# Kernel tuning notes

Measured on AMD Instinct MI355X. Metric: run time of the kernel, lower is better.

Reference implementation:

```python
import jax, jax.numpy as jnp
import numpy as np

DIM = 1536
NH = 12
HD = DIM // NH  # 128
FF, HH, WW = 32, 8, 12
L = FF * HH * WW  # 3072
WIN = (8, 4, 4)  # block of 128 tokens
BLK = WIN[0] * WIN[1] * WIN[2]


def rms_norm(x, g, eps=1e-5):
    # matches RMSNorm: normalize in fp32, scale by weight
    v = jnp.mean(jnp.square(x), axis=-1, keepdims=True)
    return x * jax.lax.rsqrt(v + eps) * g


def rope(x, freqs, n):
    # x: [B,S,D]; freqs: [S,1,HD/2,2] (cos,sin); complex rotation on pairs
    B, S, D = x.shape
    xr = x.reshape(B, S, n, D // n // 2, 2)
    c, s = freqs[..., 0], freqs[..., 1]        # [S,1,HD/2] broadcast over B,n
    a, b = xr[..., 0], xr[..., 1]
    out = jnp.stack([a * c - b * s, a * s + b * c], axis=-1)
    return out.reshape(B, S, D)


def partition3d(x, f, h, w):
    # [B,f,h,w,D] -> [B, nblocks, 128, D], block order (f/8, h/4, w/4)
    B, D = x.shape[0], x.shape[-1]
    wf, wh, ww = WIN
    x = x.reshape(B, f // wf, wf, h // wh, wh, w // ww, ww, D)
    x = x.transpose(0, 1, 3, 5, 2, 4, 6, 7)
    return x.reshape(B, -1, BLK, D)


def reverse3d(xw, f, h, w):
    # [B, nblocks, 128, D] -> [B, f*h*w, D]
    B, D = xw.shape[0], xw.shape[-1]
    wf, wh, ww = WIN
    x = xw.reshape(B, f // wf, h // wh, w // ww, wf, wh, ww, D)
    x = x.transpose(0, 1, 4, 2, 5, 3, 6, 7)
    return x.reshape(B, f * h * w, D)


def block_mask(f, h, w):
    # build_local_block_mask_3d: spatial mask is all-ones; temporal = context|local
    seqlen = f // WIN[0]
    nb_sp = (h // WIN[1]) * (w // WIN[2])
    stride = WIN[0]
    ctx_idx = (6 + stride - 1) // stride - 1          # context_frames=6
    radius = (5 + stride - 1) // stride               # temp_window_frames=5
    t = jnp.arange(seqlen)
    mt = (t[None, :] <= ctx_idx) | (jnp.abs(t[:, None] - t[None, :]) <= radius)
    # expand temporal block mask over spatial blocks -> [nb, nb]
    return jnp.repeat(jnp.repeat(mt, nb_sp, axis=0), nb_sp, axis=1)


def setup_inputs() -> dict:
    key = jax.random.key(0)
    ks = jax.random.split(key, 8)
    x = jax.random.normal(ks[0], (1, L, DIM), jnp.float32)
    ang = jax.random.uniform(ks[1], (L, 1, HD // 2), jnp.float32, 0.0, 2.0 * np.pi)
    freqs = jnp.stack([jnp.cos(ang), jnp.sin(ang)], axis=-1)  # [L,1,64,2]
    sc = 1.0 / np.sqrt(DIM)
    Wq = jax.random.normal(ks[2], (DIM, DIM), jnp.float32) * sc
    Wk = jax.random.normal(ks[3], (DIM, DIM), jnp.float32) * sc
    Wv = jax.random.normal(ks[4], (DIM, DIM), jnp.float32) * sc
    Wo = jax.random.normal(ks[5], (DIM, DIM), jnp.float32) * sc
    zeros = jnp.zeros((DIM,), jnp.float32)
    ones = jnp.ones((DIM,), jnp.float32)
    return {"x": x, "freqs": freqs, "Wq": Wq, "bq": zeros, "Wk": Wk, "bk": zeros,
            "Wv": Wv, "bv": zeros, "Wo": Wo, "bo": zeros, "g_q": ones, "g_k": ones,
            "f": FF, "h": HH, "w": WW, "local_range": 18}


def reference(x, freqs, Wq, bq, Wk, bk, Wv, bv, Wo, bo, g_q, g_k, f, h, w, local_range):
    B, S, D = x.shape
    q = rms_norm(x @ Wq + bq, g_q, eps=1e-5)
    k = rms_norm(x @ Wk + bk, g_k, eps=1e-5)
    v = x @ Wv + bv
    q = rope(q, freqs, NH)
    k = rope(k, freqs, NH)
    # window partition and flatten back to a reordered sequence
    qs = partition3d(q.reshape(B, f, h, w, D), f, h, w).reshape(B, S, D)
    ks_ = partition3d(k.reshape(B, f, h, w, D), f, h, w).reshape(B, S, D)
    vs = partition3d(v.reshape(B, f, h, w, D), f, h, w).reshape(B, S, D)
    bm = block_mask(f, h, w)                       # [nb, nb] bool
    tok_mask = jnp.repeat(jnp.repeat(bm, BLK, 0), BLK, 1)  # [S, S]
    qh = qs.reshape(B, S, NH, HD).transpose(0, 2, 1, 3)
    kh = ks_.reshape(B, S, NH, HD).transpose(0, 2, 1, 3)
    vh = vs.reshape(B, S, NH, HD).transpose(0, 2, 1, 3)
    scores = jnp.einsum('bhqd,bhkd->bhqk', qh, kh) / np.sqrt(HD)
    scores = jnp.where(tok_mask[None, None], scores, -jnp.inf)
    attn = jax.nn.softmax(scores, axis=-1)
    out = jnp.einsum('bhqk,bhkd->bhqd', attn, vh)
    out = out.transpose(0, 2, 1, 3).reshape(B, S, D)
    out = reverse3d(out.reshape(B, -1, BLK, D), f, h, w)  # undo window reorder
    return out @ Wo + bo
```

## Files before the change

kernel.cpp:

```cpp
#include <hip/hip_runtime.h>
#include <hip/hip_bf16.h>
#include <math.h>

#define S_LEN 3072
#define DMODEL 1536
#define NQKV 4608
#define NHEAD 12
#define HDIM 128
#define NSPLIT 4

typedef __attribute__((ext_vector_type(8))) short bf16x8;
typedef __attribute__((ext_vector_type(4))) float f32x4;
typedef __attribute__((ext_vector_type(4))) unsigned int u32x4;

__device__ __forceinline__ void gload_lds16(const void* g, void* lds) {
  __builtin_amdgcn_global_load_lds(
      (const __attribute__((address_space(1))) unsigned int*)g,
      (__attribute__((address_space(3))) unsigned int*)lds, 16, 0, 0);
}

__device__ __forceinline__ int invperm(int p) {
  int blk = p >> 7;
  int w   = p & 127;
  int fb  = blk / 6;
  int rem = blk - fb * 6;
  int hb  = rem / 3;
  int wb  = rem - hb * 3;
  int fi  = fb * 8 + (w >> 4);
  int hi  = hb * 4 + ((w >> 2) & 3);
  int wi  = wb * 4 + (w & 3);
  return (fi * 8 + hi) * 12 + wi;
}

__device__ __forceinline__ int fwdperm(int s) {
  int fi = s / 96;
  int rem = s - fi * 96;
  int hi = rem / 12;
  int wi = rem - hi * 12;
  int fb = fi >> 3, wf = fi & 7;
  int hb = hi >> 2, wh = hi & 3;
  int wb = wi >> 2, ww = wi & 3;
  return ((fb * 2 + hb) * 3 + wb) * 128 + wf * 16 + wh * 4 + ww;
}

__device__ __forceinline__ void store_out(float* p, float v) { *p = v; }
__device__ __forceinline__ void store_out(__hip_bfloat16* p, float v) { *p = __float2bfloat16(v); }

__global__ __launch_bounds__(256) void convert_bias(
    const float* __restrict__ in, __hip_bfloat16* __restrict__ out,
    const float* __restrict__ bq, const float* __restrict__ bk,
    const float* __restrict__ bv, float* __restrict__ bqkv)
{
  if (blockIdx.x < 4608) {
    int i = blockIdx.x * 256 + threadIdx.x;
    float4 v = ((const float4*)in)[i];
    __hip_bfloat16 b[4] = {__float2bfloat16(v.x), __float2bfloat16(v.y),
                           __float2bfloat16(v.z), __float2bfloat16(v.w)};
    ((ushort4*)out)[i] = *(ushort4*)b;
  } else {
    int j = (blockIdx.x - 4608) * 256 + threadIdx.x;
    float v = (j < 1536) ? bq[j] : (j < 3072) ? bk[j - 1536] : bv[j - 3072];
    bqkv[j] = v;
  }
}

__global__ __launch_bounds__(256) void transpose_convert4(
    const float* __restrict__ W0, const float* __restrict__ W1,
    const float* __restrict__ W2, const float* __restrict__ W3,
    __hip_bfloat16* __restrict__ Wtqkv, __hip_bfloat16* __restrict__ Wot)
{
  __shared__ __hip_bfloat16 Ls[64][67];
  const int z = blockIdx.z;
  const float* W = (z == 0) ? W0 : (z == 1) ? W1 : (z == 2) ? W2 : W3;
  __hip_bfloat16* Wt = (z < 3) ? Wtqkv + (size_t)z * DMODEL * DMODEL : Wot;
  const int r0 = blockIdx.y * 64, c0 = blockIdx.x * 64, t = threadIdx.x;
  {
    int rr = t >> 2, cb = (t & 3) * 16;
    const float4* src = (const float4*)(W + (size_t)(r0 + rr) * DMODEL + c0 + cb);
    #pragma unroll
    for (int i = 0; i < 4; ++i) {
      float4 v = src[i];
      Ls[rr][cb + i * 4 + 0] = __float2bfloat16(v.x);
      Ls[rr][cb + i * 4 + 1] = __float2bfloat16(v.y);
      Ls[rr][cb + i * 4 + 2] = __float2bfloat16(v.z);
      Ls[rr][cb + i * 4 + 3] = __float2bfloat16(v.w);
    }
  }
  __syncthreads();
  {
    int cc = t >> 2, rb = (t & 3) * 16;
    unsigned short tmp[16];
    #pragma unroll
    for (int i = 0; i < 16; ++i) tmp[i] = *(unsigned short*)&Ls[rb + i][cc];
    uint4* dst = (uint4*)(Wt + (size_t)(c0 + cc) * DMODEL + r0 + rb);
    dst[0] = ((uint4*)tmp)[0];
    dst[1] = ((uint4*)tmp)[1];
  }
}

template <typename OutT, int BN>
__global__ __launch_bounds__(256) void gemm_bt(
    const __hip_bfloat16* __restrict__ A, const __hip_bfloat16* __restrict__ Bt,
    const float* __restrict__ bias, OutT* __restrict__ C, int M, int N, int K)
{
  constexpr int NB = BN / 32;
  __shared__ __hip_bfloat16 As[2][128 * 32];
  __shared__ __hip_bfloat16 Bs[2][BN * 32];
  const int tid = threadIdx.x, lane = tid & 63, wid = tid >> 6;
  const int l15 = lane & 15, l4 = lane >> 4;
  const int nwg = gridDim.x * gridDim.y;
  const int lin = blockIdx.y * gridDim.x + blockIdx.x;
  const int cpx = nwg >> 3;
  const int swz = (lin & 7) * cpx + (lin >> 3);
  const int row0 = (swz / gridDim.x) * 128, col0 = (swz % gridDim.x) * BN;
  const int wr = (wid >> 1) * 64, wc = (wid & 1) * (BN / 2);

  f32x4 acc[4][NB] = {};
  const char* Ab = (const char*)A;
  const char* Bb = (const char*)Bt;

  auto STAGE = [&](int buf, int k0) {
    #pragma unroll
    for (int i = 0; i < 2; ++i) {
      int slot = i * 256 + tid;
      int r = slot >> 2;
      int b = (slot & 3) * 16;
      gload_lds16(Ab + ((size_t)(row0 + r) * K + k0) * 2 + b,
                  (char*)As[buf] + ((size_t)i * 256 + wid * 64) * 16);
    }
    #pragma unroll
    for (int i = 0; i < BN / 64; ++i) {
      int slot = i * 256 + tid;
      int r = slot >> 2;
      int b = (slot & 3) * 16;
      gload_lds16(Bb + ((size_t)(col0 + r) * K + k0) * 2 + b,
                  (char*)Bs[buf] + ((size_t)i * 256 + wid * 64) * 16);
    }
  };

  STAGE(0, 0);
  __syncthreads();
  int cur = 0;
  for (int k0 = 0; k0 < K; k0 += 32) {
    if (k0 + 32 < K) STAGE(cur ^ 1, k0 + 32);
    bf16x8 a[4], b[NB];
    #pragma unroll
    for (int m = 0; m < 4; ++m)
      a[m] = *(const bf16x8*)&As[cur][(wr + m * 16 + l15) * 32 + l4 * 8];
    #pragma unroll
    for (int n = 0; n < NB; ++n)
      b[n] = *(const bf16x8*)&Bs[cur][(wc + n * 16 + l15) * 32 + l4 * 8];
    #pragma unroll
    for (int m = 0; m < 4; ++m)
      #pragma unroll
      for (int n = 0; n < NB; ++n)
        acc[m][n] = __builtin_amdgcn_mfma_f32_16x16x32_bf16(a[m], b[n], acc[m][n], 0, 0, 0);
    __syncthreads();
    cur ^= 1;
  }

  #pragma unroll
  for (int m = 0; m < 4; ++m) {
    #pragma unroll
    for (int r = 0; r < 4; ++r) {
      size_t row = row0 + wr + m * 16 + l4 * 4 + r;
      #pragma unroll
      for (int n = 0; n < NB; ++n) {
        int col = col0 + wc + n * 16 + l15;
        store_out(&C[row * N + col], acc[m][n][r] + bias[col]);
      }
    }
  }
}

__global__ __launch_bounds__(256) void norm_rope_perm(
    const __hip_bfloat16* __restrict__ X,
    const float* __restrict__ gq, const float* __restrict__ gk,
    const float* __restrict__ freqs,
    __hip_bfloat16* __restrict__ OutQ, __hip_bfloat16* __restrict__ OutK)
{
  const int s = blockIdx.x, tid = threadIdx.x;
  const int sec = blockIdx.y;
  const float* g = sec ? gk : gq;
  __hip_bfloat16* Out = sec ? OutK : OutQ;
  const float qsc = sec ? 1.0f : (0.08838834764831843f * 1.4426950408889634f);
  const unsigned int* row = (const unsigned int*)(X + (size_t)s * NQKV + sec * 1536);
  float e0[3], e1[3];
  float ss = 0.f;
  #pragma unroll
  for (int i = 0; i < 3; ++i) {
    unsigned int u = row[tid + i * 256];
    float a = __uint_as_float(u << 16);
    float b = __uint_as_float(u & 0xffff0000u);
    e0[i] = a; e1[i] = b;
    ss += a * a + b * b;
  }
  #pragma unroll
  for (int off = 32; off > 0; off >>= 1) ss += __shfl_down(ss, off, 64);
  __shared__ float wsum[4];
  if ((tid & 63) == 0) wsum[tid >> 6] = ss;
  __syncthreads();
  float rs = rsqrtf((wsum[0] + wsum[1] + wsum[2] + wsum[3]) * (1.f / DMODEL) + 1e-5f);
  rs *= qsc;
  const int p = fwdperm(s);
  #pragma unroll
  for (int i = 0; i < 3; ++i) {
    int pi = tid + i * 256;
    int n = pi >> 6, d2 = pi & 63;
    float c  = freqs[(size_t)s * 128 + 2 * d2];
    float sn = freqs[(size_t)s * 128 + 2 * d2 + 1];
    float y0 = e0[i] * rs * g[2 * pi];
    float y1 = e1[i] * rs * g[2 * pi + 1];
    float o0 = y0 * c - y1 * sn;
    float o1 = y0 * sn + y1 * c;
    __hip_bfloat16 b0 = __float2bfloat16(o0), b1 = __float2bfloat16(o1);
    unsigned int u = ((unsigned int)(*(unsigned short*)&b1) << 16) | (*(unsigned short*)&b0);
    ((unsigned int*)Out)[(((size_t)n * S_LEN + p) * HDIM + 2 * d2) >> 1] = u;
  }
}

__global__ __launch_bounds__(256) void v_transpose(
    const __hip_bfloat16* __restrict__ Vsec, __hip_bfloat16* __restrict__ Vt)
{
  __shared__ __hip_bfloat16 Ls[64][136];
  const int p0 = blockIdx.x * 64, h = blockIdx.y, t = threadIdx.x;
  {
    int pl = t & 63, dg = t >> 6;
    int sidx = invperm(p0 + pl);
    const uint4* src = (const uint4*)(Vsec + (size_t)sidx * NQKV + h * HDIM + dg * 32);
    #pragma unroll
    for (int i = 0; i < 4; ++i) {
      uint4 v = src[i];
      *(uint4*)&Ls[pl][dg * 32 + i * 8] = v;
    }
  }
  __syncthreads();
  {
    int d = t >> 1, ph = t & 1;
    unsigned short tmp[32];
    #pragma unroll
    for (int i = 0; i < 32; ++i) tmp[i] = *(unsigned short*)&Ls[ph * 32 + i][d];
    uint4* dst = (uint4*)(Vt + ((size_t)h * HDIM + d) * S_LEN + p0 + ph * 32);
    #pragma unroll
    for (int i = 0; i < 4; ++i) dst[i] = ((uint4*)tmp)[i];
  }
}

__global__ __launch_bounds__(512) void attn_mfma(
    const __hip_bfloat16* __restrict__ Qp, const __hip_bfloat16* __restrict__ Kp,
    const __hip_bfloat16* __restrict__ Vt,
    __hip_bfloat16* __restrict__ Opart, float* __restrict__ ml)
{
  __shared__ __hip_bfloat16 Ks[64 * 128];
  __shared__ __hip_bfloat16 Vs[128 * 64];

  const int hw = blockIdx.x + 24 * (blockIdx.y + NSPLIT * blockIdx.z);
  const int L  = (hw & 7) * 144 + (hw >> 3);
  const int j  = L % 6;
  const int t4 = (L / 6) & 3;
  const int sh = L / 24;
  const int h  = sh % 12;
  const int split = sh / 12;
  const int tg = (t4 == 0) ? 2 : (t4 == 1) ? 1 : (t4 == 2) ? 3 : 0;
  const int qb = tg * 6 + j;

  const int tid = threadIdx.x, lane = tid & 63, wid = tid >> 6;
  const int l15 = lane & 15, l4 = lane >> 4;

  const int NCh = (tg == 0) ? 6 : (tg == 2) ? 12 : 9;
  const int cbegin = split * NCh, cend = cbegin + NCh;

  const char* Kh = (const char*)(Kp + (size_t)h * S_LEN * HDIM);
  const char* Vh = (const char*)(Vt + (size_t)h * HDIM * S_LEN);

  const int kbase = 8 * (l15 >> 2) + (l15 & 3);
  const int ksw = (((l15 & 3) | (((l15 >> 2) & 1) << 2))) << 4;

  unsigned int koffA, voffA;
  {
    unsigned int kr = tid >> 4;
    unsigned int sig = (kr & 3) | (((kr >> 3) & 1) << 2);
    koffA = kr * 256 + (((tid & 15) * 16) ^ (sig << 4));
    unsigned int vr = tid >> 3;
    voffA = vr * (S_LEN * 2) + (((tid & 7) * 16) ^ ((vr & 7) << 4));
  }

  auto k0_of = [&](int ci) { return ci * 64 + ((tg == 3 && ci >= 12) ? 768 : 0); };
  auto STAGE = [&](int k0) {
    const char* ks = Kh + (size_t)k0 * 256;
    gload_lds16(ks + koffA,        (char*)Ks + tid * 16);
    gload_lds16(ks + koffA + 8192, (char*)Ks + tid * 16 + 8192);
    const char* vs = Vh + (size_t)k0 * 2 + voffA;
    gload_lds16(vs,                          (char*)Vs + tid * 16);
    gload_lds16(vs + (size_t)64 * S_LEN * 2, (char*)Vs + tid * 16 + 8192);
  };

  bf16x8 aq[4];
  {
    const __hip_bfloat16* qr = Qp + (size_t)h * S_LEN * HDIM
        + (size_t)(qb * 128 + wid * 16 + l15) * HDIM + l4 * 8;
    #pragma unroll
    for (int dc = 0; dc < 4; ++dc) aq[dc] = *(const bf16x8*)(qr + dc * 32);
  }

  f32x4 oacc[8] = {};
  float m2 = -1e30f;
  float lsum = 0.f;

  for (int ci = cbegin; ci < cend; ++ci) {
    const int k0 = k0_of(ci);
    STAGE(k0);
    __syncthreads();

    f32x4 sfr[4] = {};
    #pragma unroll
    for (int ct = 0; ct < 4; ++ct) {
      int key = kbase + (ct >> 1) * 32 + (ct & 1) * 4;
      #pragma unroll
      for (int dc = 0; dc < 4; ++dc) {
        int b = (dc * 64 + l4 * 16) ^ ksw;
        bf16x8 kf = *(const bf16x8*)((const char*)Ks + key * 256 + b);
        sfr[ct] = __builtin_amdgcn_mfma_f32_16x16x32_bf16(kf, aq[dc], sfr[ct], 0, 0, 0);
      }
    }
    float lmax = fmaxf(
        fmaxf(fmaxf(sfr[0][0], sfr[0][1]), fmaxf(sfr[0][2], sfr[0][3])),
        fmaxf(fmaxf(fmaxf(sfr[1][0], sfr[1][1]), fmaxf(sfr[1][2], sfr[1][3])),
              fmaxf(fmaxf(fmaxf(sfr[2][0], sfr[2][1]), fmaxf(sfr[2][2], sfr[2][3])),
                    fmaxf(fmaxf(sfr[3][0], sfr[3][1]), fmaxf(sfr[3][2], sfr[3][3])))));
    bool grow = lmax > m2 + 8.f;
    if (ci == cbegin || __any(grow)) {
      float mf = lmax;
      mf = fmaxf(mf, __shfl_xor(mf, 16, 64));
      mf = fmaxf(mf, __shfl_xor(mf, 32, 64));
      float mn = fmaxf(m2, mf);
      float corr = exp2f(m2 - mn);
      m2 = mn;
      lsum *= corr;
      float cr[4];
      #pragma unroll
      for (int r = 0; r < 4; ++r) cr[r] = __shfl(corr, l4 * 4 + r, 64);
      #pragma unroll
      for (int n = 0; n < 8; ++n)
        #pragma unroll
        for (int r = 0; r < 4; ++r) oacc[n][r] *= cr[r];
    }
    #pragma unroll
    for (int ct = 0; ct < 4; ++ct)
      #pragma unroll
      for (int r = 0; r < 4; ++r) {
        float p = exp2f(sfr[ct][r] - m2);
        sfr[ct][r] = p;
        lsum += p;
      }
    #pragma unroll
    for (int ks = 0; ks < 2; ++ks) {
      u32x4 wv;
      {
        __hip_bfloat16 a0 = __float2bfloat16(sfr[2 * ks][0]);
        __hip_bfloat16 a1 = __float2bfloat16(sfr[2 * ks][1]);
        __hip_bfloat16 a2 = __float2bfloat16(sfr[2 * ks][2]);
        __hip_bfloat16 a3 = __float2bfloat16(sfr[2 * ks][3]);
        __hip_bfloat16 b0 = __float2bfloat16(sfr[2 * ks + 1][0]);
        __hip_bfloat16 b1 = __float2bfloat16(sfr[2 * ks + 1][1]);
        __hip_bfloat16 b2 = __float2bfloat16(sfr[2 * ks + 1][2]);
        __hip_bfloat16 b3 = __float2bfloat16(sfr[2 * ks + 1][3]);
        wv[0] = ((unsigned int)(*(unsigned short*)&a1) << 16) | (*(unsigned short*)&a0);
        wv[1] = ((unsigned int)(*(unsigned short*)&a3) << 16) | (*(unsigned short*)&a2);
        wv[2] = ((unsigned int)(*(unsigned short*)&b1) << 16) | (*(unsigned short*)&b0);
        wv[3] = ((unsigned int)(*(unsigned short*)&b3) << 16) | (*(unsigned short*)&b2);
      }
      bf16x8 pa = __builtin_bit_cast(bf16x8, wv);
      #pragma unroll
      for (int n = 0; n < 8; ++n) {
        int d = n * 16 + l15;
        int b = (ks * 64 + l4 * 16) ^ ((d & 7) << 4);
        bf16x8 bv = *(const bf16x8*)((const char*)Vs + d * 128 + b);
        oacc[n] = __builtin_amdgcn_mfma_f32_16x16x32_bf16(pa, bv, oacc[n], 0, 0, 0);
      }
    }
    __syncthreads();
  }

  float t = lsum;
  t += __shfl_xor(t, 16, 64);
  t += __shfl_xor(t, 32, 64);
  float inv = 1.0f / t;
  #pragma unroll
  for (int r = 0; r < 4; ++r) {
    float invr = __shfl(inv, l4 * 4 + r, 64);
    int qrow = qb * 128 + wid * 16 + l4 * 4 + r;
    size_t rowid = (size_t)(split * NHEAD + h) * S_LEN + qrow;
    __hip_bfloat16* dst = Opart + rowid * HDIM;
    #pragma unroll
    for (int n = 0; n < 8; ++n)
      dst[n * 16 + l15] = __float2bfloat16(oacc[n][r] * invr);
  }
  if (lane < 16) {
    int qrow = qb * 128 + wid * 16 + lane;
    size_t rowid = (size_t)(split * NHEAD + h) * S_LEN + qrow;
    ml[rowid * 2 + 0] = m2;
    ml[rowid * 2 + 1] = t;
  }
}

__global__ __launch_bounds__(256) void attn_merge(
    const __hip_bfloat16* __restrict__ Opart, const float* __restrict__ ml,
    __hip_bfloat16* __restrict__ AO)
{
  const int rid = blockIdx.x * 4 + (threadIdx.x >> 6);
  const int lane = threadIdx.x & 63;
  const int h = rid / S_LEN, q = rid - h * S_LEN;
  size_t rr[NSPLIT];
  float m[NSPLIT], l[NSPLIT];
  float mm = -1e30f;
  #pragma unroll
  for (int s = 0; s < NSPLIT; ++s) {
    rr[s] = (size_t)(s * NHEAD + h) * S_LEN + q;
    m[s] = ml[rr[s] * 2];
    l[s] = ml[rr[s] * 2 + 1];
    mm = fmaxf(mm, m[s]);
  }
  float wsum = 0.f, wgt[NSPLIT];
  #pragma unroll
  for (int s = 0; s < NSPLIT; ++s) { wgt[s] = l[s] * exp2f(m[s] - mm); wsum += wgt[s]; }
  float inv = 1.0f / wsum;
  float o0 = 0.f, o1 = 0.f;
  #pragma unroll
  for (int s = 0; s < NSPLIT; ++s) {
    unsigned int u = ((const unsigned int*)(Opart + rr[s] * HDIM))[lane];
    float a = wgt[s] * inv;
    o0 += a * __uint_as_float(u << 16);
    o1 += a * __uint_as_float(u & 0xffff0000u);
  }
  __hip_bfloat16 b0 = __float2bfloat16(o0), b1 = __float2bfloat16(o1);
  unsigned int u = ((unsigned int)(*(unsigned short*)&b1) << 16) | (*(unsigned short*)&b0);
  int sorig = invperm(q);
  ((unsigned int*)(AO + (size_t)sorig * DMODEL + h * HDIM))[lane] = u;
}

extern "C" void kernel_launch(void* const* d_in, const int* in_sizes, int n_in,
                              void* d_out, int out_size, void* d_ws, size_t ws_size,
                              hipStream_t stream)
{
  (void)in_sizes; (void)n_in; (void)out_size; (void)ws_size;
  const float* x     = (const float*)d_in[0];
  const float* freqs = (const float*)d_in[1];
  const float* Wq    = (const float*)d_in[2];
  const float* bq    = (const float*)d_in[3];
  const float* Wk    = (const float*)d_in[4];
  const float* bk    = (const float*)d_in[5];
  const float* Wv    = (const float*)d_in[6];
  const float* bv    = (const float*)d_in[7];
  const float* Wo    = (const float*)d_in[8];
  const float* bo    = (const float*)d_in[9];
  const float* gq    = (const float*)d_in[10];
  const float* gk    = (const float*)d_in[11];
  float* out = (float*)d_out;

  char* w = (char*)d_ws;
  __hip_bfloat16* xbf    = (__hip_bfloat16*)(w);
  __hip_bfloat16* Wtqkv  = (__hip_bfloat16*)(w + 9437184);
  __hip_bfloat16* QKVbf  = (__hip_bfloat16*)(w + 23592960);
  __hip_bfloat16* Qp     = (__hip_bfloat16*)(w + 51904512);
  __hip_bfloat16* Kp     = (__hip_bfloat16*)(w + 61341696);
  __hip_bfloat16* Vtb    = (__hip_bfloat16*)(w + 70778880);
  __hip_bfloat16* AO     = (__hip_bfloat16*)(w + 80216064);
  __hip_bfloat16* Wot    = (__hip_bfloat16*)(w + 89653248);
  float*          bqkv   = (float*)(w + 94371840);
  __hip_bfloat16* Opart  = (__hip_bfloat16*)(w + 9437184);
  float*          mlbuf  = (float*)(w);

  hipLaunchKernelGGL(convert_bias, dim3(4626), dim3(256), 0, stream,
                     x, xbf, bq, bk, bv, bqkv);
  hipLaunchKernelGGL(transpose_convert4, dim3(24, 24, 4), dim3(256), 0, stream,
                     Wq, Wk, Wv, Wo, Wtqkv, Wot);

  hipLaunchKernelGGL((gemm_bt<__hip_bfloat16, 128>), dim3(NQKV / 128, S_LEN / 128),
                     dim3(256), 0, stream, xbf, Wtqkv, bqkv, QKVbf, S_LEN, NQKV, DMODEL);

  hipLaunchKernelGGL(norm_rope_perm, dim3(S_LEN, 2), dim3(256), 0, stream,
                     QKVbf, gq, gk, freqs, Qp, Kp);
  hipLaunchKernelGGL(v_transpose, dim3(48, 12), dim3(256), 0, stream, QKVbf + 3072, Vtb);

  hipLaunchKernelGGL(attn_mfma, dim3(24, NSPLIT, NHEAD), dim3(512), 0, stream,
                     Qp, Kp, Vtb, Opart, mlbuf);
  hipLaunchKernelGGL(attn_merge, dim3(S_LEN * NHEAD / 4), dim3(256), 0, stream,
                     Opart, mlbuf, AO);

  hipLaunchKernelGGL((gemm_bt<float, 64>), dim3(DMODEL / 64, S_LEN / 128),
                     dim3(256), 0, stream, AO, Wot, bo, out, S_LEN, DMODEL, DMODEL);
}
```

Measured before the change: 227.9 us.

## Retile QKV GEMM, remap XCD swizzle, relax GEMM barriers, prioritize attention MFMA

The GEMM workgroup mapping now gives each XCD a contiguous 2D sub-tile of the output grid, which should improve L2 reuse. The per-iteration __syncthreads is replaced with partial s_waitcnt vmcnt plus raw barriers, so the next stage's loads can stay in flight while the current tile is consumed. The QKV GEMM switches from 128-wide to 64-wide N tiles to launch more workgroups. The attention kernel raises wave priority around its MFMA blocks with s_setprio. The vmcnt counts are hand-tuned to the number of loads per stage, so they are fragile, and the mapping assumes grid dimensions divisible by 4 and 2.

```diff
diff --git a/kernel.cpp b/kernel.cpp
--- a/kernel.cpp
+++ b/kernel.cpp
@@ -108,11 +108,12 @@
   __shared__ __hip_bfloat16 Bs[2][BN * 32];
   const int tid = threadIdx.x, lane = tid & 63, wid = tid >> 6;
   const int l15 = lane & 15, l4 = lane >> 4;
-  const int nwg = gridDim.x * gridDim.y;
   const int lin = blockIdx.y * gridDim.x + blockIdx.x;
-  const int cpx = nwg >> 3;
-  const int swz = (lin & 7) * cpx + (lin >> 3);
-  const int row0 = (swz / gridDim.x) * 128, col0 = (swz % gridDim.x) * BN;
+  const int xcd = lin & 7, idx = lin >> 3;
+  const int CX = gridDim.x >> 2, CY = gridDim.y >> 1;
+  const int cx = xcd & 3, cy = xcd >> 2;
+  const int lc = idx % CX, lr = idx / CX;
+  const int row0 = (cy * CY + lr) * 128, col0 = (cx * CX + lc) * BN;
   const int wr = (wid >> 1) * 64, wc = (wid & 1) * (BN / 2);
 
   f32x4 acc[4][NB] = {};
@@ -139,10 +140,21 @@
   };
 
   STAGE(0, 0);
-  __syncthreads();
+  asm volatile("s_waitcnt vmcnt(0)" ::: "memory");
+  __builtin_amdgcn_s_barrier();
+  __builtin_amdgcn_sched_barrier(0);
+
   int cur = 0;
   for (int k0 = 0; k0 < K; k0 += 32) {
-    if (k0 + 32 < K) STAGE(cur ^ 1, k0 + 32);
+    if (k0 + 32 < K) {
+      STAGE(cur ^ 1, k0 + 32);
+      if constexpr (BN == 64)
+        asm volatile("s_waitcnt vmcnt(3)" ::: "memory");
+      else
+        asm volatile("s_waitcnt vmcnt(4)" ::: "memory");
+      __builtin_amdgcn_s_barrier();
+    }
+    __builtin_amdgcn_sched_barrier(0);
     bf16x8 a[4], b[NB];
     #pragma unroll
     for (int m = 0; m < 4; ++m)
@@ -155,7 +167,8 @@
       #pragma unroll
       for (int n = 0; n < NB; ++n)
         acc[m][n] = __builtin_amdgcn_mfma_f32_16x16x32_bf16(a[m], b[n], acc[m][n], 0, 0, 0);
-    __syncthreads();
+    __builtin_amdgcn_sched_barrier(0);
+    __builtin_amdgcn_s_barrier();
     cur ^= 1;
   }
 
@@ -313,6 +326,7 @@
     __syncthreads();
 
     f32x4 sfr[4] = {};
+    __builtin_amdgcn_s_setprio(1);
     #pragma unroll
     for (int ct = 0; ct < 4; ++ct) {
       int key = kbase + (ct >> 1) * 32 + (ct & 1) * 4;
@@ -323,6 +337,7 @@
         sfr[ct] = __builtin_amdgcn_mfma_f32_16x16x32_bf16(kf, aq[dc], sfr[ct], 0, 0, 0);
       }
     }
+    __builtin_amdgcn_s_setprio(0);
     float lmax = fmaxf(
         fmaxf(fmaxf(sfr[0][0], sfr[0][1]), fmaxf(sfr[0][2], sfr[0][3])),
         fmaxf(fmaxf(fmaxf(sfr[1][0], sfr[1][1]), fmaxf(sfr[1][2], sfr[1][3])),
@@ -371,6 +386,7 @@
         wv[3] = ((unsigned int)(*(unsigned short*)&b3) << 16) | (*(unsigned short*)&b2);
       }
       bf16x8 pa = __builtin_bit_cast(bf16x8, wv);
+      __builtin_amdgcn_s_setprio(1);
       #pragma unroll
       for (int n = 0; n < 8; ++n) {
         int d = n * 16 + l15;
@@ -378,6 +394,7 @@
         bf16x8 bv = *(const bf16x8*)((const char*)Vs + d * 128 + b);
         oacc[n] = __builtin_amdgcn_mfma_f32_16x16x32_bf16(pa, bv, oacc[n], 0, 0, 0);
       }
+      __builtin_amdgcn_s_setprio(0);
     }
     __syncthreads();
   }
@@ -476,7 +493,7 @@
   hipLaunchKernelGGL(transpose_convert4, dim3(24, 24, 4), dim3(256), 0, stream,
                      Wq, Wk, Wv, Wo, Wtqkv, Wot);
 
-  hipLaunchKernelGGL((gemm_bt<__hip_bfloat16, 128>), dim3(NQKV / 128, S_LEN / 128),
+  hipLaunchKernelGGL((gemm_bt<__hip_bfloat16, 64>), dim3(NQKV / 64, S_LEN / 128),
                      dim3(256), 0, stream, xbf, Wtqkv, bqkv, QKVbf, S_LEN, NQKV, DMODEL);
 
   hipLaunchKernelGGL(norm_rope_perm, dim3(S_LEN, 2), dim3(256), 0, stream,
```

New measurement: 229.2 us. No clear change (+0.6%).
